# Performance work log

Measured on AMD Instinct MI355X. Metric: run time of the kernel, lower is better.

## Reference

```python
import jax, jax.numpy as jnp
import numpy as np

DEPTH, BREADTH, N_HEADS = 6, 1024, 16
D_HEAD = BREADTH // N_HEADS
EPS = 1e-5


def layer_norm(x, g, b):
    m = jnp.mean(x, axis=-1, keepdims=True)
    v = jnp.mean(jnp.square(x - m), axis=-1, keepdims=True)
    return (x - m) * jax.lax.rsqrt(v + EPS) * g + b


def setup_inputs() -> dict:
    key = jax.random.key(0)
    ks = jax.random.split(key, 16)
    B, S, Dm, Dff = 4, 1024, BREADTH, 4 * BREADTH
    s = 0.02
    return {
        "x": jax.random.normal(ks[0], (B, S, Dm), dtype=jnp.float32),
        "mask": jnp.ones((B, S, S), dtype=jnp.int32),
        "wq": s * jax.random.normal(ks[1], (DEPTH, Dm, Dm), dtype=jnp.float32),
        "bq": jnp.zeros((DEPTH, Dm), dtype=jnp.float32),
        "wk": s * jax.random.normal(ks[2], (DEPTH, Dm, Dm), dtype=jnp.float32),
        "bk": jnp.zeros((DEPTH, Dm), dtype=jnp.float32),
        "wv": s * jax.random.normal(ks[3], (DEPTH, Dm, Dm), dtype=jnp.float32),
        "bv": jnp.zeros((DEPTH, Dm), dtype=jnp.float32),
        "wo": s * jax.random.normal(ks[4], (DEPTH, Dm, Dm), dtype=jnp.float32),
        "bo": jnp.zeros((DEPTH, Dm), dtype=jnp.float32),
        "w1": s * jax.random.normal(ks[5], (DEPTH, Dm, Dff), dtype=jnp.float32),
        "b1": jnp.zeros((DEPTH, Dff), dtype=jnp.float32),
        "w2": s * jax.random.normal(ks[6], (DEPTH, Dff, Dm), dtype=jnp.float32),
        "b2": jnp.zeros((DEPTH, Dm), dtype=jnp.float32),
        "ln1g": jnp.ones((DEPTH, Dm), dtype=jnp.float32),
        "ln1b": jnp.zeros((DEPTH, Dm), dtype=jnp.float32),
        "ln2g": jnp.ones((DEPTH, Dm), dtype=jnp.float32),
        "ln2b": jnp.zeros((DEPTH, Dm), dtype=jnp.float32),
        "lnfg": jnp.ones((Dm,), dtype=jnp.float32),
        "lnfb": jnp.zeros((Dm,), dtype=jnp.float32),
    }


def reference(x, mask, wq, bq, wk, bk, wv, bv, wo, bo, w1, b1, w2, b2,
              ln1g, ln1b, ln2g, ln2b, lnfg, lnfb):
    B, S, Dm = x.shape
    scale = 1.0 / jnp.sqrt(jnp.float32(D_HEAD))
    neg = jnp.float32(-1e9)
    mask_b = (mask == 0)[:, None]  # [B,1,S,S]

    def split_heads(t):  # [B,S,Dm] -> [B,H,S,d]
        return t.reshape(B, S, N_HEADS, D_HEAD).transpose(0, 2, 1, 3)

    for i in range(DEPTH):
        xn1 = layer_norm(x, ln1g[i], ln1b[i])  # attention branch input
        xn2 = layer_norm(x, ln2g[i], ln2b[i])  # FFN branch input (pre-attention, per original)

        q = split_heads(xn1 @ wq[i] + bq[i])
        k = split_heads(xn1 @ wk[i] + bk[i])
        v = split_heads(xn1 @ wv[i] + bv[i])
        scores = jnp.einsum("bhqd,bhkd->bhqk", q, k) * scale
        scores = jnp.where(mask_b, neg, scores)
        attn = jax.nn.softmax(scores, axis=-1)
        ctx = jnp.einsum("bhqk,bhkd->bhqd", attn, v)
        ctx = ctx.transpose(0, 2, 1, 3).reshape(B, S, Dm)
        x = x + (ctx @ wo[i] + bo[i])

        h = jax.nn.relu(xn2 @ w1[i] + b1[i])
        x = x + (h @ w2[i] + b2[i])

    return layer_norm(x, lnfg, lnfb)
```

## Files before the change

### kernel.cpp

```cpp
#include <hip/hip_runtime.h>
#include <hip/hip_bf16.h>
#include <stdint.h>

#define DEPTH 6
#define DM 1024
#define DFF 4096
#define NH 16
#define DH 64
#define BATCH 4
#define SEQ 1024
#define NTOK (BATCH*SEQ)
#define QKVLD 3072

using bf16x8 = __attribute__((ext_vector_type(8))) short;
using f32x4  = __attribute__((ext_vector_type(4))) float;
typedef unsigned short u16;

__device__ __forceinline__ u16 f2bf(float f) {
  union { float f; uint32_t u; } v; v.f = f;
  return (u16)((v.u + 0x7FFFu + ((v.u >> 16) & 1u)) >> 16);
}

__device__ __forceinline__ void async16(void* lds, const void* g) {
  __builtin_amdgcn_global_load_lds(
      (__attribute__((address_space(1))) void*)(unsigned long long)g,
      (__attribute__((address_space(3))) void*)(unsigned int)(unsigned long long)lds,
      16, 0, 0);
}

__global__ __launch_bounds__(256)
void prep(const float* __restrict__ wq, const float* __restrict__ wk,
          const float* __restrict__ wv, const float* __restrict__ wo,
          const float* __restrict__ w1, const float* __restrict__ w2,
          const float* __restrict__ bq, const float* __restrict__ bk,
          const float* __restrict__ bv,
          u16* __restrict__ wqkvT, u16* __restrict__ woT,
          u16* __restrict__ w1T, u16* __restrict__ w2T,
          float* __restrict__ bqkv) {
  const int bid = blockIdx.x;
  if (bid >= 12288) {
    const int t = (bid - 12288) * 256 + threadIdx.x;
    bqkv[t] = t < 1024 ? bq[t] : (t < 2048 ? bk[t - 1024] : bv[t - 2048]);
    return;
  }
  const float* w; u16* wt; int K, N, tile;
  if (bid < 3072)      { const int r = bid >> 10;
                         w = r == 0 ? wq : (r == 1 ? wk : wv);
                         wt = wqkvT + (size_t)r * 1024 * 1024; K = 1024; N = 1024; tile = bid & 1023; }
  else if (bid < 4096) { w = wo; wt = woT; K = 1024; N = 1024; tile = bid - 3072; }
  else if (bid < 8192) { w = w1; wt = w1T; K = 1024; N = 4096; tile = bid - 4096; }
  else                 { w = w2; wt = w2T; K = 4096; N = 1024; tile = bid - 8192; }
  const int ntn = N >> 5;
  const int k0 = (tile / ntn) << 5, n0 = (tile % ntn) << 5;

  __shared__ u16 t[32][33];
  const int tx = threadIdx.x & 31, ty = threadIdx.x >> 5;
  #pragma unroll
  for (int r = ty; r < 32; r += 8)
    t[r][tx] = f2bf(w[(size_t)(k0 + r) * N + n0 + tx]);
  __syncthreads();
  #pragma unroll
  for (int r = ty; r < 32; r += 8)
    wt[(size_t)(n0 + r) * K + k0 + tx] = t[tx][r];
}

__global__ __launch_bounds__(256)
void vtrans(const u16* __restrict__ qkv, u16* __restrict__ vt) {
  __shared__ u16 t[64][72];
  const int s0 = blockIdx.x * 64, c0 = blockIdx.y * 64, b = blockIdx.z;
  const int r = threadIdx.x >> 2, cq = threadIdx.x & 3;
  const u16* src = qkv + ((size_t)(b * SEQ + s0 + r)) * QKVLD + 2048 + c0 + cq * 16;
  *(bf16x8*)&t[r][cq * 16]     = *(const bf16x8*)(src);
  *(bf16x8*)&t[r][cq * 16 + 8] = *(const bf16x8*)(src + 8);
  __syncthreads();
  bf16x8 a, bvec;
  #pragma unroll
  for (int i = 0; i < 8; i++) a[i] = (short)t[cq * 16 + i][r];
  #pragma unroll
  for (int i = 0; i < 8; i++) bvec[i] = (short)t[cq * 16 + 8 + i][r];
  u16* dst = vt + ((size_t)(b * 1024 + c0 + r)) * SEQ + s0 + cq * 16;
  *(bf16x8*)dst = a;
  *(bf16x8*)(dst + 8) = bvec;
}

__global__ void flags_init(int* flags) {
  if (threadIdx.x < BATCH) flags[threadIdx.x] = 1;
}
__global__ void mask_flags(const int* __restrict__ mask, int* __restrict__ flags) {
  const size_t n = (size_t)BATCH * SEQ * SEQ;
  for (size_t i = (size_t)blockIdx.x * 256 + threadIdx.x; i < n; i += (size_t)gridDim.x * 256)
    if (mask[i] == 0) flags[i / ((size_t)SEQ * SEQ)] = 0;
}

__global__ __launch_bounds__(256)
void ln_dual(const float* __restrict__ x,
             const float* __restrict__ g1, const float* __restrict__ b1v,
             const float* __restrict__ g2, const float* __restrict__ b2v,
             u16* __restrict__ o1, u16* __restrict__ o2) {
  const int row = blockIdx.x, tid = threadIdx.x;
  const float4 v = ((const float4*)(x + (size_t)row * DM))[tid];
  float s = v.x + v.y + v.z + v.w;
  float sq = v.x*v.x + v.y*v.y + v.z*v.z + v.w*v.w;
  #pragma unroll
  for (int o = 32; o; o >>= 1) { s += __shfl_xor(s, o); sq += __shfl_xor(sq, o); }
  __shared__ float red[8];
  const int lane = tid & 63, w = tid >> 6;
  if (lane == 0) { red[w] = s; red[4 + w] = sq; }
  __syncthreads();
  s = red[0] + red[1] + red[2] + red[3];
  sq = red[4] + red[5] + red[6] + red[7];
  const float mean = s * (1.0f / DM);
  const float rinv = rsqrtf(sq * (1.0f / DM) - mean * mean + 1e-5f);
  const float4 G1 = ((const float4*)g1)[tid], B1 = ((const float4*)b1v)[tid];
  const float4 G2 = ((const float4*)g2)[tid], B2 = ((const float4*)b2v)[tid];
  const float n0 = (v.x - mean) * rinv, n1 = (v.y - mean) * rinv;
  const float n2 = (v.z - mean) * rinv, n3 = (v.w - mean) * rinv;
  ushort4 a, bb;
  a.x = f2bf(n0*G1.x + B1.x); a.y = f2bf(n1*G1.y + B1.y);
  a.z = f2bf(n2*G1.z + B1.z); a.w = f2bf(n3*G1.w + B1.w);
  bb.x = f2bf(n0*G2.x + B2.x); bb.y = f2bf(n1*G2.y + B2.y);
  bb.z = f2bf(n2*G2.z + B2.z); bb.w = f2bf(n3*G2.w + B2.w);
  ((ushort4*)(o1 + (size_t)row * DM))[tid] = a;
  ((ushort4*)(o2 + (size_t)row * DM))[tid] = bb;
}

__global__ __launch_bounds__(256)
void ln_final(const float* __restrict__ x, const float* __restrict__ g,
              const float* __restrict__ b, float* __restrict__ out) {
  const int row = blockIdx.x, tid = threadIdx.x;
  const float4 v = ((const float4*)(x + (size_t)row * DM))[tid];
  float s = v.x + v.y + v.z + v.w;
  float sq = v.x*v.x + v.y*v.y + v.z*v.z + v.w*v.w;
  #pragma unroll
  for (int o = 32; o; o >>= 1) { s += __shfl_xor(s, o); sq += __shfl_xor(sq, o); }
  __shared__ float red[8];
  const int lane = tid & 63, w = tid >> 6;
  if (lane == 0) { red[w] = s; red[4 + w] = sq; }
  __syncthreads();
  s = red[0] + red[1] + red[2] + red[3];
  sq = red[4] + red[5] + red[6] + red[7];
  const float mean = s * (1.0f / DM);
  const float rinv = rsqrtf(sq * (1.0f / DM) - mean * mean + 1e-5f);
  const float4 G = ((const float4*)g)[tid], B = ((const float4*)b)[tid];
  float4 o;
  o.x = (v.x - mean) * rinv * G.x + B.x;
  o.y = (v.y - mean) * rinv * G.y + B.y;
  o.z = (v.z - mean) * rinv * G.z + B.z;
  o.w = (v.w - mean) * rinv * G.w + B.w;
  ((float4*)(out + (size_t)row * DM))[tid] = o;
}

template<int EPI, int BN>
__global__ __launch_bounds__(256)
void gemm_bt(const u16* __restrict__ A, const u16* __restrict__ BT,
             const float* __restrict__ bias,
             u16* __restrict__ Cb, float* __restrict__ Cf,
             int M, int N, int K) {
  constexpr int WCn = BN / 64;
  constexpr int WR  = 4 / WCn;
  constexpr int MF  = 8 / WR;
  constexpr int WRS = 128 / WR;
  constexpr int ASZ = 128 * 32;
  constexpr int BSZ = BN * 32;
  __shared__ u16 As[2 * ASZ];
  __shared__ u16 Bs[2 * BSZ];
  const int tid = threadIdx.x;
  const int lane = tid & 63, wave = tid >> 6;
  const int wr = wave / WCn, wc = wave % WCn;
  const int l16 = lane & 15, lhi = lane >> 4;

  const int ntn = N / BN;
  const int nwg = (M >> 7) * ntn;
  int wg = (int)blockIdx.x;
  if ((nwg & 7) == 0) { const int q = nwg >> 3; wg = (wg & 7) * q + (wg >> 3); }
  const int tm = wg / ntn, tn = wg % ntn;

  const int srow = tid >> 2, sc = (tid & 3) * 8;
  const u16* Ag0 = A  + (size_t)(tm * 128 + srow) * K + sc;
  const u16* Bg0 = BT + (size_t)(tn * BN + srow) * K + sc;
  const size_t rstep = (size_t)64 * K;

  auto stage = [&](int buf, int k0) {
    async16(As + buf * ASZ + tid * 8, Ag0 + k0);
    async16(As + buf * ASZ + 2048 + tid * 8, Ag0 + rstep + k0);
    async16(Bs + buf * BSZ + tid * 8, Bg0 + k0);
    if constexpr (BN == 128) async16(Bs + buf * BSZ + 2048 + tid * 8, Bg0 + rstep + k0);
  };

  f32x4 acc[MF][4];
  #pragma unroll
  for (int m = 0; m < MF; m++)
    #pragma unroll
    for (int n = 0; n < 4; n++)
      #pragma unroll
      for (int j = 0; j < 4; j++) acc[m][n][j] = 0.0f;

  stage(0, 0);
  __syncthreads();
  int cur = 0;
  for (int k0 = 0; k0 < K; k0 += 32) {
    if (k0 + 32 < K) stage(cur ^ 1, k0 + 32);
    const u16* Ab = As + cur * ASZ;
    const u16* Bb = Bs + cur * BSZ;
    bf16x8 af[MF], bfv[4];
    #pragma unroll
    for (int m = 0; m < MF; m++)
      af[m] = *(const bf16x8*)&Ab[(wr * WRS + m * 16 + l16) * 32 + lhi * 8];
    #pragma unroll
    for (int n = 0; n < 4; n++)
      bfv[n] = *(const bf16x8*)&Bb[(wc * 64 + n * 16 + l16) * 32 + lhi * 8];
    #pragma unroll
    for (int m = 0; m < MF; m++)
      #pragma unroll
      for (int n = 0; n < 4; n++)
        acc[m][n] = __builtin_amdgcn_mfma_f32_16x16x32_bf16(af[m], bfv[n], acc[m][n], 0, 0, 0);
    __syncthreads();
    cur ^= 1;
  }

  const int row0 = tm * 128 + wr * WRS + lhi * 4;
  const int col0 = tn * BN + wc * 64 + l16;
  #pragma unroll
  for (int n = 0; n < 4; n++) {
    const int col = col0 + n * 16;
    const float bv = bias[col];
    #pragma unroll
    for (int m = 0; m < MF; m++) {
      #pragma unroll
      for (int j = 0; j < 4; j++) {
        const int row = row0 + m * 16 + j;
        float v = acc[m][n][j] + bv;
        if constexpr (EPI == 1) v = fmaxf(v, 0.0f);
        if constexpr (EPI <= 1) Cb[(size_t)row * N + col] = f2bf(v);
        else                    Cf[(size_t)row * N + col] += v;
      }
    }
  }
}

__global__ __launch_bounds__(256, 4)
void attn(const u16* __restrict__ QKV, const u16* __restrict__ VTg,
          u16* __restrict__ Octx,
          const int* __restrict__ mask, const int* __restrict__ flags) {
  __shared__ u16 Ks[2 * 64 * 64];
  __shared__ u16 VTs[2 * 64 * 64];
  __shared__ u16 Ps[4 * 16 * 64];
  const int tid = threadIdx.x, lane = tid & 63, wv = tid >> 6;
  const int l16 = lane & 15, lhi = lane >> 4;
  const int bid = blockIdx.x;
  const int pair = bid >> 4, qblk = bid & 15;
  const int b = pair >> 4, h = pair & 15;
  const int hoff = h * DH;
  const int q0 = qblk * 64 + wv * 16;
  const size_t tokbase = (size_t)b * SEQ;
  const size_t vbase = ((size_t)b * 1024 + hoff) * SEQ;

  bf16x8 qf[2];
  #pragma unroll
  for (int ds = 0; ds < 2; ds++)
    qf[ds] = *(const bf16x8*)&QKV[(tokbase + q0 + l16) * QKVLD + hoff + ds * 32 + lhi * 8];

  f32x4 oacc[4];
  #pragma unroll
  for (int nt = 0; nt < 4; nt++)
    #pragma unroll
    for (int j = 0; j < 4; j++) oacc[nt][j] = 0.0f;
  float mrun = -1e30f, lrun = 0.0f;

  const int allone = flags[b];
  char* PwB = (char*)(Ps + wv * (16 * 64));
  const int xw = (l16 & 7) << 4;

  const int srow0 = tid >> 3, scb0 = (tid & 7) ^ (srow0 & 7);
  const int srow1 = (tid + 256) >> 3, scb1 = (tid & 7) ^ (srow1 & 7);
  const int shfl_src = (lane & 48) + ((lane >> 4) << 2);

  auto stage = [&](int buf, int kt) {
    async16((char*)Ks + buf * 8192 + tid * 16,
            &QKV[(tokbase + kt + srow0) * QKVLD + 1024 + hoff + scb0 * 8]);
    async16((char*)Ks + buf * 8192 + 4096 + tid * 16,
            &QKV[(tokbase + kt + srow1) * QKVLD + 1024 + hoff + scb1 * 8]);
    async16((char*)VTs + buf * 8192 + tid * 16,
            &VTg[vbase + (size_t)srow0 * SEQ + kt + scb0 * 8]);
    async16((char*)VTs + buf * 8192 + 4096 + tid * 16,
            &VTg[vbase + (size_t)srow1 * SEQ + kt + scb1 * 8]);
  };

  stage(0, 0);
  __syncthreads();
  int cur = 0;
  for (int kt = 0; kt < SEQ; kt += 64) {
    if (kt + 64 < SEQ) stage(cur ^ 1, kt + 64);
    char* KsB = (char*)Ks + cur * 8192;
    char* VTB = (char*)VTs + cur * 8192;

    f32x4 sacc[4];
    #pragma unroll
    for (int nt = 0; nt < 4; nt++)
      #pragma unroll
      for (int j = 0; j < 4; j++) sacc[nt][j] = 0.0f;
    #pragma unroll
    for (int ds = 0; ds < 2; ds++) {
      bf16x8 kf[4];
      #pragma unroll
      for (int nt = 0; nt < 4; nt++) {
        const int rk = nt * 16 + l16;
        kf[nt] = *(const bf16x8*)(KsB + ((rk * 128 + ds * 64 + lhi * 16) ^ ((rk & 7) << 4)));
      }
      #pragma unroll
      for (int nt = 0; nt < 4; nt++)
        sacc[nt] = __builtin_amdgcn_mfma_f32_16x16x32_bf16(kf[nt], qf[ds], sacc[nt], 0, 0, 0);
    }
    #pragma unroll
    for (int nt = 0; nt < 4; nt++)
      #pragma unroll
      for (int j = 0; j < 4; j++) sacc[nt][j] *= 0.125f;

    if (!allone) {
      const int qg = q0 + l16;
      #pragma unroll
      for (int nt = 0; nt < 4; nt++)
        #pragma unroll
        for (int j = 0; j < 4; j++) {
          const int kc = kt + nt * 16 + lhi * 4 + j;
          if (mask[(tokbase + qg) * SEQ + kc] == 0) sacc[nt][j] = -1e9f;
        }
    }

    float tmax = -1e30f;
    #pragma unroll
    for (int nt = 0; nt < 4; nt++)
      #pragma unroll
      for (int j = 0; j < 4; j++) tmax = fmaxf(tmax, sacc[nt][j]);
    tmax = fmaxf(tmax, __shfl_xor(tmax, 16));
    tmax = fmaxf(tmax, __shfl_xor(tmax, 32));
    const float mnew = fmaxf(mrun, tmax);
    const float corr = __expf(mrun - mnew);
    float p[4][4];
    float tsum = 0.0f;
    #pragma unroll
    for (int nt = 0; nt < 4; nt++)
      #pragma unroll
      for (int j = 0; j < 4; j++) { p[nt][j] = __expf(sacc[nt][j] - mnew); tsum += p[nt][j]; }
    tsum += __shfl_xor(tsum, 16);
    tsum += __shfl_xor(tsum, 32);
    lrun = lrun * corr + tsum;
    mrun = mnew;

    #pragma unroll
    for (int nt = 0; nt < 4; nt++) {
      const uint32_t lo = (uint32_t)f2bf(p[nt][0]) | ((uint32_t)f2bf(p[nt][1]) << 16);
      const uint32_t hi = (uint32_t)f2bf(p[nt][2]) | ((uint32_t)f2bf(p[nt][3]) << 16);
      *(uint64_t*)(PwB + ((l16 * 128 + nt * 32 + lhi * 8) ^ xw)) =
          (uint64_t)lo | ((uint64_t)hi << 32);
    }

    float cj[4];
    #pragma unroll
    for (int j = 0; j < 4; j++) cj[j] = __shfl(corr, shfl_src + j);
    #pragma unroll
    for (int nt = 0; nt < 4; nt++)
      #pragma unroll
      for (int j = 0; j < 4; j++) oacc[nt][j] *= cj[j];

    #pragma unroll
    for (int ksl = 0; ksl < 2; ksl++) {
      const bf16x8 pf = *(const bf16x8*)(PwB + ((l16 * 128 + ksl * 64 + lhi * 16) ^ xw));
      #pragma unroll
      for (int nt = 0; nt < 4; nt++) {
        const int dr = nt * 16 + l16;
        const bf16x8 vf = *(const bf16x8*)(VTB + ((dr * 128 + ksl * 64 + lhi * 16) ^ ((dr & 7) << 4)));
        oacc[nt] = __builtin_amdgcn_mfma_f32_16x16x32_bf16(pf, vf, oacc[nt], 0, 0, 0);
      }
    }
    __syncthreads();
    cur ^= 1;
  }

  const float linv = 1.0f / lrun;
  float lj[4];
  #pragma unroll
  for (int j = 0; j < 4; j++) lj[j] = __shfl(linv, shfl_src + j);
  #pragma unroll
  for (int j = 0; j < 4; j++) {
    const size_t rowg = (tokbase + q0 + lhi * 4 + j) * DM + hoff;
    #pragma unroll
    for (int nt = 0; nt < 4; nt++)
      Octx[rowg + nt * 16 + l16] = f2bf(oacc[nt][j] * lj[j]);
  }
}

extern "C" void kernel_launch(void* const* d_in, const int* in_sizes, int n_in,
                              void* d_out, int out_size, void* d_ws, size_t ws_size,
                              hipStream_t stream) {
  const float* x    = (const float*)d_in[0];
  const int*   mask = (const int*)d_in[1];
  const float* wq = (const float*)d_in[2];
  const float* bq = (const float*)d_in[3];
  const float* wk = (const float*)d_in[4];
  const float* bk = (const float*)d_in[5];
  const float* wvp = (const float*)d_in[6];
  const float* bv = (const float*)d_in[7];
  const float* wo = (const float*)d_in[8];
  const float* bo = (const float*)d_in[9];
  const float* w1 = (const float*)d_in[10];
  const float* b1 = (const float*)d_in[11];
  const float* w2 = (const float*)d_in[12];
  const float* b2 = (const float*)d_in[13];
  const float* ln1g = (const float*)d_in[14];
  const float* ln1b = (const float*)d_in[15];
  const float* ln2g = (const float*)d_in[16];
  const float* ln2b = (const float*)d_in[17];
  const float* lnfg = (const float*)d_in[18];
  const float* lnfb = (const float*)d_in[19];

  char* ws = (char*)d_ws;
  float* xbuf = (float*)(ws);
  u16* xn1  = (u16*)(ws + ((size_t)16 << 20));
  u16* xn2  = (u16*)(ws + ((size_t)24 << 20));
  u16* qkv  = (u16*)(ws + ((size_t)32 << 20));
  u16* ctx  = (u16*)(ws + ((size_t)56 << 20));
  u16* hb   = (u16*)(ws + ((size_t)32 << 20));
  u16* wqkvT= (u16*)(ws + ((size_t)64 << 20));
  u16* woT  = (u16*)(ws + ((size_t)70 << 20));
  u16* w1T  = (u16*)(ws + ((size_t)72 << 20));
  u16* w2T  = (u16*)(ws + ((size_t)80 << 20));
  u16* vT   = (u16*)(ws + ((size_t)88 << 20));
  float* bqkv = (float*)(ws + ((size_t)96 << 20));
  int* flags  = (int*)(ws + ((size_t)96 << 20) + 65536);

  hipMemcpyAsync(xbuf, x, (size_t)NTOK * DM * sizeof(float),
                 hipMemcpyDeviceToDevice, stream);
  flags_init<<<1, 64, 0, stream>>>(flags);
  mask_flags<<<1024, 256, 0, stream>>>(mask, flags);

  auto wgs128 = [](int M, int N) { return dim3((unsigned)((M >> 7) * (N >> 7))); };
  auto wgs64  = [](int M, int N) { return dim3((unsigned)((M >> 7) * (N >> 6))); };

  for (int i = 0; i < DEPTH; i++) {
    prep<<<12300, 256, 0, stream>>>(
        wq  + (size_t)i * DM * DM,  wk + (size_t)i * DM * DM,
        wvp + (size_t)i * DM * DM,  wo + (size_t)i * DM * DM,
        w1  + (size_t)i * DM * DFF, w2 + (size_t)i * DFF * DM,
        bq + i * DM, bk + i * DM, bv + i * DM,
        wqkvT, woT, w1T, w2T, bqkv);

    ln_dual<<<NTOK, 256, 0, stream>>>(xbuf, ln1g + i * DM, ln1b + i * DM,
                                      ln2g + i * DM, ln2b + i * DM, xn1, xn2);

    gemm_bt<0, 128><<<wgs128(NTOK, QKVLD), 256, 0, stream>>>(xn1, wqkvT, bqkv, qkv, nullptr,
                                                             NTOK, QKVLD, DM);
    vtrans<<<dim3(16, 16, 4), 256, 0, stream>>>(qkv, vT);

    attn<<<1024, 256, 0, stream>>>(qkv, vT, ctx, mask, flags);

    gemm_bt<2, 64><<<wgs64(NTOK, DM), 256, 0, stream>>>(ctx, woT, bo + i * DM, nullptr, xbuf,
                                                        NTOK, DM, DM);
    gemm_bt<1, 128><<<wgs128(NTOK, DFF), 256, 0, stream>>>(xn2, w1T, b1 + i * DFF, hb, nullptr,
                                                           NTOK, DFF, DM);
    gemm_bt<2, 64><<<wgs64(NTOK, DM), 256, 0, stream>>>(hb, w2T, b2 + i * DM, nullptr, xbuf,
                                                        NTOK, DM, DFF);
  }

  ln_final<<<NTOK, 256, 0, stream>>>(xbuf, lnfg, lnfb, (float*)d_out);
}
```

Before: 1.523 ms.

## Add 256x256 tiled bf16 GEMM with split-K atomics for QKV and FFN layers

Introduces a new 512-thread GEMM kernel with 256x256 output tiles, a swizzled LDS layout, double-buffered async global-to-LDS loads, interleaved MFMA phases with priority hints, and XCD-aware workgroup remapping. It replaces the 128-tile GEMMs for the QKV and FFN-up projections. The FFN-down projection now uses 4-way split-K with float atomic adds into the residual buffer. The larger tiles aim to raise arithmetic intensity and cut global and LDS traffic per MFMA. In exchange, atomic accumulation makes the floating-point sum order nondeterministic, and register pressure from the 8x4 accumulator tile is high.

After: 1.591 ms. +4.4%, slower.

```diff
diff --git a/kernel.cpp b/kernel.cpp
--- a/kernel.cpp
+++ b/kernel.cpp
@@ -27,6 +27,8 @@
       (__attribute__((address_space(3))) void*)(unsigned int)(unsigned long long)lds,
       16, 0, 0);
 }
+
+#define BARRIER() do { __builtin_amdgcn_s_barrier(); asm volatile("" ::: "memory"); } while (0)
 
 __global__ __launch_bounds__(256)
 void prep(const float* __restrict__ wq, const float* __restrict__ wk,
@@ -148,6 +150,176 @@
   o.z = (v.z - mean) * rinv * G.z + B.z;
   o.w = (v.w - mean) * rinv * G.w + B.w;
   ((float4*)(out + (size_t)row * DM))[tid] = o;
+}
+
+template<int EPI, int SPLITK>
+__global__ __launch_bounds__(512, 2)
+void gemm256(const u16* __restrict__ A, const u16* __restrict__ BT,
+             const float* __restrict__ bias,
+             u16* __restrict__ Cb, float* __restrict__ Cf,
+             int M, int N, int K) {
+  __shared__ u16 lds[65536];
+  char* ldsb = (char*)lds;
+  const int tid = threadIdx.x;
+  const int lane = tid & 63;
+  const int wid = tid >> 6;
+  const int wm = wid >> 2, wn = wid & 3;
+  const int l16 = lane & 15, lhi = lane >> 4;
+  const int xr = (l16 & 7) << 4;
+
+  const int ntn = N >> 8;
+  const int ntiles = (M >> 8) * ntn;
+  const int nwg = ntiles * SPLITK;
+  int wg = (int)blockIdx.x;
+  if ((nwg & 7) == 0) { const int q = nwg >> 3; wg = (wg & 7) * q + (wg >> 3); }
+  const int ks = wg / ntiles;
+  const int tile = wg % ntiles;
+  const int tm = tile / ntn, tn = tile % ntn;
+  const int KS = K / SPLITK;
+  const int k0 = ks * KS;
+  const int NT = KS >> 6;
+
+  const u16 *aS[4], *bS[4];
+  #pragma unroll
+  for (int g = 0; g < 4; g++) {
+    const int D  = tid * 16 + g * 8192;
+    const int Dh = D & 16383, half = D >> 14;
+    const int Ds = Dh ^ (((Dh >> 7) & 7) << 4);
+    const int grow = half * 128 + (Ds >> 7);
+    const int gcol = (Ds & 127) >> 1;
+    aS[g] = A  + (size_t)(tm * 256 + grow) * K + k0 + gcol;
+    bS[g] = BT + (size_t)(tn * 256 + grow) * K + k0 + gcol;
+  }
+  auto stageA = [&](int buf, int t) {
+    #pragma unroll
+    for (int g = 0; g < 4; g++)
+      async16(ldsb + buf * 32768 + g * 8192 + tid * 16, aS[g] + t * 64);
+  };
+  auto stageB = [&](int buf, int t) {
+    #pragma unroll
+    for (int g = 0; g < 4; g++)
+      async16(ldsb + 65536 + buf * 32768 + g * 8192 + tid * 16, bS[g] + t * 64);
+  };
+  auto ldA = [&](int buf, int mq, int m, int kk) -> bf16x8 {
+    const int L = (mq * 64 + m * 16 + l16) * 128 + kk * 64 + lhi * 16;
+    return *(const bf16x8*)(ldsb + buf * 32768 + wm * 16384 + (L ^ xr));
+  };
+  auto ldB = [&](int buf, int nq, int n, int kk) -> bf16x8 {
+    const int L = ((wn & 1) * 64 + nq * 32 + n * 16 + l16) * 128 + kk * 64 + lhi * 16;
+    return *(const bf16x8*)(ldsb + 65536 + buf * 32768 + (wn >> 1) * 16384 + (L ^ xr));
+  };
+
+  f32x4 acc[8][4];
+  #pragma unroll
+  for (int m = 0; m < 8; m++)
+    #pragma unroll
+    for (int n = 0; n < 4; n++)
+      #pragma unroll
+      for (int j = 0; j < 4; j++) acc[m][n][j] = 0.0f;
+
+  stageA(0, 0); stageB(0, 0);
+  stageA(1, 1); stageB(1, 1);
+  asm volatile("s_waitcnt vmcnt(8)" ::: "memory");
+  BARRIER();
+
+  bf16x8 a[4][2], b0[2][2], b1[2][2];
+  for (int t = 0; t < NT; ++t) {
+    const int buf = t & 1;
+    #pragma unroll
+    for (int m = 0; m < 4; m++)
+      #pragma unroll
+      for (int kk = 0; kk < 2; kk++) a[m][kk] = ldA(buf, 0, m, kk);
+    #pragma unroll
+    for (int n = 0; n < 2; n++)
+      #pragma unroll
+      for (int kk = 0; kk < 2; kk++) b0[n][kk] = ldB(buf, 0, n, kk);
+    BARRIER();
+    asm volatile("s_waitcnt lgkmcnt(0)" ::: "memory");
+    __builtin_amdgcn_s_setprio(1);
+    #pragma unroll
+    for (int m = 0; m < 4; m++)
+      #pragma unroll
+      for (int n = 0; n < 2; n++)
+        #pragma unroll
+        for (int kk = 0; kk < 2; kk++)
+          acc[m][n] = __builtin_amdgcn_mfma_f32_16x16x32_bf16(a[m][kk], b0[n][kk], acc[m][n], 0, 0, 0);
+    __builtin_amdgcn_s_setprio(0);
+    BARRIER();
+    #pragma unroll
+    for (int n = 0; n < 2; n++)
+      #pragma unroll
+      for (int kk = 0; kk < 2; kk++) b1[n][kk] = ldB(buf, 1, n, kk);
+    BARRIER();
+    asm volatile("s_waitcnt lgkmcnt(0)" ::: "memory");
+    __builtin_amdgcn_s_setprio(1);
+    #pragma unroll
+    for (int m = 0; m < 4; m++)
+      #pragma unroll
+      for (int n = 0; n < 2; n++)
+        #pragma unroll
+        for (int kk = 0; kk < 2; kk++)
+          acc[m][2 + n] = __builtin_amdgcn_mfma_f32_16x16x32_bf16(a[m][kk], b1[n][kk], acc[m][2 + n], 0, 0, 0);
+    __builtin_amdgcn_s_setprio(0);
+    BARRIER();
+    #pragma unroll
+    for (int m = 0; m < 4; m++)
+      #pragma unroll
+      for (int kk = 0; kk < 2; kk++) a[m][kk] = ldA(buf, 1, m, kk);
+    if (t + 2 < NT) stageB(buf, t + 2);
+    BARRIER();
+    asm volatile("s_waitcnt lgkmcnt(0)" ::: "memory");
+    __builtin_amdgcn_s_setprio(1);
+    #pragma unroll
+    for (int m = 0; m < 4; m++)
+      #pragma unroll
+      for (int n = 0; n < 2; n++)
+        #pragma unroll
+        for (int kk = 0; kk < 2; kk++)
+          acc[4 + m][2 + n] = __builtin_amdgcn_mfma_f32_16x16x32_bf16(a[m][kk], b1[n][kk], acc[4 + m][2 + n], 0, 0, 0);
+    __builtin_amdgcn_s_setprio(0);
+    BARRIER();
+    if (t + 2 < NT) stageA(buf, t + 2);
+    BARRIER();
+    __builtin_amdgcn_s_setprio(1);
+    #pragma unroll
+    for (int m = 0; m < 4; m++)
+      #pragma unroll
+      for (int n = 0; n < 2; n++)
+        #pragma unroll
+        for (int kk = 0; kk < 2; kk++)
+          acc[4 + m][n] = __builtin_amdgcn_mfma_f32_16x16x32_bf16(a[m][kk], b0[n][kk], acc[4 + m][n], 0, 0, 0);
+    __builtin_amdgcn_s_setprio(0);
+    if (t + 1 < NT) {
+      if (t + 2 < NT) asm volatile("s_waitcnt vmcnt(8)" ::: "memory");
+      else            asm volatile("s_waitcnt vmcnt(0)" ::: "memory");
+      BARRIER();
+    }
+  }
+
+  const int row0 = tm * 256 + wm * 128 + lhi * 4;
+  const int col0 = tn * 256 + wn * 64 + l16;
+  #pragma unroll
+  for (int ng = 0; ng < 4; ng++) {
+    const int col = col0 + ng * 16;
+    const float bv = bias[col];
+    #pragma unroll
+    for (int mg = 0; mg < 8; mg++) {
+      #pragma unroll
+      for (int j = 0; j < 4; j++) {
+        const int row = row0 + mg * 16 + j;
+        float v = acc[mg][ng][j];
+        if constexpr (EPI == 2 && SPLITK > 1) {
+          if (ks == 0) v += bv;
+          unsafeAtomicAdd(&Cf[(size_t)row * N + col], v);
+        } else {
+          v += bv;
+          if constexpr (EPI == 1) v = fmaxf(v, 0.0f);
+          if constexpr (EPI <= 1) Cb[(size_t)row * N + col] = f2bf(v);
+          else                    Cf[(size_t)row * N + col] += v;
+        }
+      }
+    }
+  }
 }
 
 template<int EPI, int BN>
@@ -434,8 +606,7 @@
   flags_init<<<1, 64, 0, stream>>>(flags);
   mask_flags<<<1024, 256, 0, stream>>>(mask, flags);
 
-  auto wgs128 = [](int M, int N) { return dim3((unsigned)((M >> 7) * (N >> 7))); };
-  auto wgs64  = [](int M, int N) { return dim3((unsigned)((M >> 7) * (N >> 6))); };
+  auto wgs64 = [](int M, int N) { return dim3((unsigned)((M >> 7) * (N >> 6))); };
 
   for (int i = 0; i < DEPTH; i++) {
     prep<<<12300, 256, 0, stream>>>(
@@ -448,18 +619,18 @@
     ln_dual<<<NTOK, 256, 0, stream>>>(xbuf, ln1g + i * DM, ln1b + i * DM,
                                       ln2g + i * DM, ln2b + i * DM, xn1, xn2);
 
-    gemm_bt<0, 128><<<wgs128(NTOK, QKVLD), 256, 0, stream>>>(xn1, wqkvT, bqkv, qkv, nullptr,
-                                                             NTOK, QKVLD, DM);
+    gemm256<0, 1><<<dim3(192), 512, 0, stream>>>(xn1, wqkvT, bqkv, qkv, nullptr,
+                                                 NTOK, QKVLD, DM);
     vtrans<<<dim3(16, 16, 4), 256, 0, stream>>>(qkv, vT);
 
     attn<<<1024, 256, 0, stream>>>(qkv, vT, ctx, mask, flags);
 
     gemm_bt<2, 64><<<wgs64(NTOK, DM), 256, 0, stream>>>(ctx, woT, bo + i * DM, nullptr, xbuf,
                                                         NTOK, DM, DM);
-    gemm_bt<1, 128><<<wgs128(NTOK, DFF), 256, 0, stream>>>(xn2, w1T, b1 + i * DFF, hb, nullptr,
-                                                           NTOK, DFF, DM);
-    gemm_bt<2, 64><<<wgs64(NTOK, DM), 256, 0, stream>>>(hb, w2T, b2 + i * DM, nullptr, xbuf,
-                                                        NTOK, DM, DFF);
+    gemm256<1, 1><<<dim3(256), 512, 0, stream>>>(xn2, w1T, b1 + i * DFF, hb, nullptr,
+                                                 NTOK, DFF, DM);
+    gemm256<2, 4><<<dim3(256), 512, 0, stream>>>(hb, w2T, b2 + i * DM, nullptr, xbuf,
+                                                 NTOK, DM, DFF);
   }
 
   ln_final<<<NTOK, 256, 0, stream>>>(xbuf, lnfg, lnfb, (float*)d_out);
```

## Split-K the W2 GEMM and fold the partial sum into the next layernorm

Applied to the files above, without the earlier changes.

The FFN down-projection (K=4096) is split into two K halves, which doubles the workgroup count from 512 to 1024. The first half adds its result plus bias into the residual buffer, and the second half writes a separate fp32 slab. The next ln_dual, or ln_final after the last layer, adds the slab into the residual before normalising and writes the sum back. This is meant to improve occupancy on a tile-count-limited GEMM, at the cost of writing and reading an extra 16MB fp32 slab per layer. The split path only runs if the workspace is large enough.

New measurement: 1.520 ms (median of 2 runs). About the same (-0.2%).

```diff
diff --git a/kernel.cpp b/kernel.cpp
--- a/kernel.cpp
+++ b/kernel.cpp
@@ -93,12 +93,17 @@
 }
 
 __global__ __launch_bounds__(256)
-void ln_dual(const float* __restrict__ x,
+void ln_dual(float* __restrict__ x, const float* __restrict__ slab,
              const float* __restrict__ g1, const float* __restrict__ b1v,
              const float* __restrict__ g2, const float* __restrict__ b2v,
              u16* __restrict__ o1, u16* __restrict__ o2) {
   const int row = blockIdx.x, tid = threadIdx.x;
-  const float4 v = ((const float4*)(x + (size_t)row * DM))[tid];
+  float4 v = ((const float4*)(x + (size_t)row * DM))[tid];
+  if (slab) {
+    const float4 sv = ((const float4*)(slab + (size_t)row * DM))[tid];
+    v.x += sv.x; v.y += sv.y; v.z += sv.z; v.w += sv.w;
+    ((float4*)(x + (size_t)row * DM))[tid] = v;
+  }
   float s = v.x + v.y + v.z + v.w;
   float sq = v.x*v.x + v.y*v.y + v.z*v.z + v.w*v.w;
   #pragma unroll
@@ -125,10 +130,15 @@
 }
 
 __global__ __launch_bounds__(256)
-void ln_final(const float* __restrict__ x, const float* __restrict__ g,
-              const float* __restrict__ b, float* __restrict__ out) {
+void ln_final(const float* __restrict__ x, const float* __restrict__ slab,
+              const float* __restrict__ g, const float* __restrict__ b,
+              float* __restrict__ out) {
   const int row = blockIdx.x, tid = threadIdx.x;
-  const float4 v = ((const float4*)(x + (size_t)row * DM))[tid];
+  float4 v = ((const float4*)(x + (size_t)row * DM))[tid];
+  if (slab) {
+    const float4 sv = ((const float4*)(slab + (size_t)row * DM))[tid];
+    v.x += sv.x; v.y += sv.y; v.z += sv.z; v.w += sv.w;
+  }
   float s = v.x + v.y + v.z + v.w;
   float sq = v.x*v.x + v.y*v.y + v.z*v.z + v.w*v.w;
   #pragma unroll
@@ -150,11 +160,11 @@
   ((float4*)(out + (size_t)row * DM))[tid] = o;
 }
 
-template<int EPI, int BN>
+template<int EPI, int BN, int SPLITK>
 __global__ __launch_bounds__(256)
 void gemm_bt(const u16* __restrict__ A, const u16* __restrict__ BT,
              const float* __restrict__ bias,
-             u16* __restrict__ Cb, float* __restrict__ Cf,
+             u16* __restrict__ Cb, float* __restrict__ Cf, float* __restrict__ Cf2,
              int M, int N, int K) {
   constexpr int WCn = BN / 64;
   constexpr int WR  = 4 / WCn;
@@ -170,14 +180,17 @@
   const int l16 = lane & 15, lhi = lane >> 4;
 
   const int ntn = N / BN;
-  const int nwg = (M >> 7) * ntn;
+  const int ntiles = (M >> 7) * ntn;
+  const int nwg = ntiles * SPLITK;
   int wg = (int)blockIdx.x;
   if ((nwg & 7) == 0) { const int q = nwg >> 3; wg = (wg & 7) * q + (wg >> 3); }
-  const int tm = wg / ntn, tn = wg % ntn;
+  const int tile = wg / SPLITK, ks = wg % SPLITK;
+  const int tm = tile / ntn, tn = tile % ntn;
+  const int KL = K / SPLITK;
 
   const int srow = tid >> 2, sc = (tid & 3) * 8;
-  const u16* Ag0 = A  + (size_t)(tm * 128 + srow) * K + sc;
-  const u16* Bg0 = BT + (size_t)(tn * BN + srow) * K + sc;
+  const u16* Ag0 = A  + (size_t)(tm * 128 + srow) * K + ks * KL + sc;
+  const u16* Bg0 = BT + (size_t)(tn * BN + srow) * K + ks * KL + sc;
   const size_t rstep = (size_t)64 * K;
 
   auto stage = [&](int buf, int k0) {
@@ -198,8 +211,8 @@
   stage(0, 0);
   __syncthreads();
   int cur = 0;
-  for (int k0 = 0; k0 < K; k0 += 32) {
-    if (k0 + 32 < K) stage(cur ^ 1, k0 + 32);
+  for (int k0 = 0; k0 < KL; k0 += 32) {
+    if (k0 + 32 < KL) stage(cur ^ 1, k0 + 32);
     const u16* Ab = As + cur * ASZ;
     const u16* Bb = Bs + cur * BSZ;
     bf16x8 af[MF], bfv[4];
@@ -229,10 +242,17 @@
       #pragma unroll
       for (int j = 0; j < 4; j++) {
         const int row = row0 + m * 16 + j;
-        float v = acc[m][n][j] + bv;
-        if constexpr (EPI == 1) v = fmaxf(v, 0.0f);
-        if constexpr (EPI <= 1) Cb[(size_t)row * N + col] = f2bf(v);
-        else                    Cf[(size_t)row * N + col] += v;
+        const size_t idx = (size_t)row * N + col;
+        float v = acc[m][n][j];
+        if constexpr (EPI == 3) {
+          if (ks == 0) Cf[idx] += v + bv;
+          else         Cf2[idx] = v;
+        } else {
+          v += bv;
+          if constexpr (EPI == 1) v = fmaxf(v, 0.0f);
+          if constexpr (EPI <= 1) Cb[idx] = f2bf(v);
+          else                    Cf[idx] += v;
+        }
       }
     }
   }
@@ -428,6 +448,9 @@
   u16* vT   = (u16*)(ws + ((size_t)88 << 20));
   float* bqkv = (float*)(ws + ((size_t)96 << 20));
   int* flags  = (int*)(ws + ((size_t)96 << 20) + 65536);
+  float* slab = (float*)(ws + ((size_t)97 << 20));
+
+  const bool splitw2 = ws_size >= ((size_t)113 << 20);
 
   hipMemcpyAsync(xbuf, x, (size_t)NTOK * DM * sizeof(float),
                  hipMemcpyDeviceToDevice, stream);
@@ -445,22 +468,30 @@
         bq + i * DM, bk + i * DM, bv + i * DM,
         wqkvT, woT, w1T, w2T, bqkv);
 
-    ln_dual<<<NTOK, 256, 0, stream>>>(xbuf, ln1g + i * DM, ln1b + i * DM,
+    ln_dual<<<NTOK, 256, 0, stream>>>(xbuf, (splitw2 && i > 0) ? slab : nullptr,
+                                      ln1g + i * DM, ln1b + i * DM,
                                       ln2g + i * DM, ln2b + i * DM, xn1, xn2);
 
-    gemm_bt<0, 128><<<wgs128(NTOK, QKVLD), 256, 0, stream>>>(xn1, wqkvT, bqkv, qkv, nullptr,
-                                                             NTOK, QKVLD, DM);
+    gemm_bt<0, 128, 1><<<wgs128(NTOK, QKVLD), 256, 0, stream>>>(
+        xn1, wqkvT, bqkv, qkv, nullptr, nullptr, NTOK, QKVLD, DM);
     vtrans<<<dim3(16, 16, 4), 256, 0, stream>>>(qkv, vT);
 
     attn<<<1024, 256, 0, stream>>>(qkv, vT, ctx, mask, flags);
 
-    gemm_bt<2, 64><<<wgs64(NTOK, DM), 256, 0, stream>>>(ctx, woT, bo + i * DM, nullptr, xbuf,
-                                                        NTOK, DM, DM);
-    gemm_bt<1, 128><<<wgs128(NTOK, DFF), 256, 0, stream>>>(xn2, w1T, b1 + i * DFF, hb, nullptr,
-                                                           NTOK, DFF, DM);
-    gemm_bt<2, 64><<<wgs64(NTOK, DM), 256, 0, stream>>>(hb, w2T, b2 + i * DM, nullptr, xbuf,
-                                                        NTOK, DM, DFF);
-  }
-
-  ln_final<<<NTOK, 256, 0, stream>>>(xbuf, lnfg, lnfb, (float*)d_out);
-}
+    gemm_bt<2, 64, 1><<<wgs64(NTOK, DM), 256, 0, stream>>>(
+        ctx, woT, bo + i * DM, nullptr, xbuf, nullptr, NTOK, DM, DM);
+    gemm_bt<1, 128, 1><<<wgs128(NTOK, DFF), 256, 0, stream>>>(
+        xn2, w1T, b1 + i * DFF, hb, nullptr, nullptr, NTOK, DFF, DM);
+
+    if (splitw2) {
+      gemm_bt<3, 64, 2><<<dim3((NTOK >> 7) * (DM >> 6) * 2), 256, 0, stream>>>(
+          hb, w2T, b2 + i * DM, nullptr, xbuf, slab, NTOK, DM, DFF);
+    } else {
+      gemm_bt<2, 64, 1><<<wgs64(NTOK, DM), 256, 0, stream>>>(
+          hb, w2T, b2 + i * DM, nullptr, xbuf, nullptr, NTOK, DM, DFF);
+    }
+  }
+
+  ln_final<<<NTOK, 256, 0, stream>>>(xbuf, splitw2 ? slab : nullptr,
+                                     lnfg, lnfb, (float*)d_out);
+}
```

## Split-K the output-projection and FFN-down GEMMs with atomic accumulation

Applied to the files above, without the earlier changes.

Adds a SPLITK template parameter to the GEMM so each workgroup covers only a slice of K, and adds an epilogue that accumulates into the fp32 residual with atomics. Bias is added only by the first slice. The Wo projection uses 2 splits and the FFN-down projection uses 4. Before this, those two N=1024 GEMMs launched only 512 workgroups, and the FFN-down one also ran a long K loop. Splitting raises workgroup count and shortens per-workgroup latency, at the cost of more atomic traffic and a summation order that is no longer deterministic.

After: 1.754 ms. +15.1%, slower.

```diff
diff --git a/kernel.cpp b/kernel.cpp
--- a/kernel.cpp
+++ b/kernel.cpp
@@ -150,7 +150,7 @@
   ((float4*)(out + (size_t)row * DM))[tid] = o;
 }
 
-template<int EPI, int BN>
+template<int EPI, int BN, int SPLITK>
 __global__ __launch_bounds__(256)
 void gemm_bt(const u16* __restrict__ A, const u16* __restrict__ BT,
              const float* __restrict__ bias,
@@ -170,14 +170,17 @@
   const int l16 = lane & 15, lhi = lane >> 4;
 
   const int ntn = N / BN;
-  const int nwg = (M >> 7) * ntn;
+  const int ntiles = (M >> 7) * ntn;
+  const int nwg = ntiles * SPLITK;
   int wg = (int)blockIdx.x;
   if ((nwg & 7) == 0) { const int q = nwg >> 3; wg = (wg & 7) * q + (wg >> 3); }
-  const int tm = wg / ntn, tn = wg % ntn;
+  const int tile = wg / SPLITK, ks = wg % SPLITK;
+  const int tm = tile / ntn, tn = tile % ntn;
+  const int KL = K / SPLITK;
 
   const int srow = tid >> 2, sc = (tid & 3) * 8;
-  const u16* Ag0 = A  + (size_t)(tm * 128 + srow) * K + sc;
-  const u16* Bg0 = BT + (size_t)(tn * BN + srow) * K + sc;
+  const u16* Ag0 = A  + (size_t)(tm * 128 + srow) * K + ks * KL + sc;
+  const u16* Bg0 = BT + (size_t)(tn * BN + srow) * K + ks * KL + sc;
   const size_t rstep = (size_t)64 * K;
 
   auto stage = [&](int buf, int k0) {
@@ -198,8 +201,8 @@
   stage(0, 0);
   __syncthreads();
   int cur = 0;
-  for (int k0 = 0; k0 < K; k0 += 32) {
-    if (k0 + 32 < K) stage(cur ^ 1, k0 + 32);
+  for (int k0 = 0; k0 < KL; k0 += 32) {
+    if (k0 + 32 < KL) stage(cur ^ 1, k0 + 32);
     const u16* Ab = As + cur * ASZ;
     const u16* Bb = Bs + cur * BSZ;
     bf16x8 af[MF], bfv[4];
@@ -229,10 +232,17 @@
       #pragma unroll
       for (int j = 0; j < 4; j++) {
         const int row = row0 + m * 16 + j;
-        float v = acc[m][n][j] + bv;
-        if constexpr (EPI == 1) v = fmaxf(v, 0.0f);
-        if constexpr (EPI <= 1) Cb[(size_t)row * N + col] = f2bf(v);
-        else                    Cf[(size_t)row * N + col] += v;
+        const size_t idx = (size_t)row * N + col;
+        float v = acc[m][n][j];
+        if constexpr (EPI == 4) {
+          if (ks == 0) v += bv;
+          unsafeAtomicAdd(&Cf[idx], v);
+        } else {
+          v += bv;
+          if constexpr (EPI == 1) v = fmaxf(v, 0.0f);
+          if constexpr (EPI <= 1) Cb[idx] = f2bf(v);
+          else                    Cf[idx] += v;
+        }
       }
     }
   }
@@ -435,7 +445,6 @@
   mask_flags<<<1024, 256, 0, stream>>>(mask, flags);
 
   auto wgs128 = [](int M, int N) { return dim3((unsigned)((M >> 7) * (N >> 7))); };
-  auto wgs64  = [](int M, int N) { return dim3((unsigned)((M >> 7) * (N >> 6))); };
 
   for (int i = 0; i < DEPTH; i++) {
     prep<<<12300, 256, 0, stream>>>(
@@ -448,18 +457,20 @@
     ln_dual<<<NTOK, 256, 0, stream>>>(xbuf, ln1g + i * DM, ln1b + i * DM,
                                       ln2g + i * DM, ln2b + i * DM, xn1, xn2);
 
-    gemm_bt<0, 128><<<wgs128(NTOK, QKVLD), 256, 0, stream>>>(xn1, wqkvT, bqkv, qkv, nullptr,
-                                                             NTOK, QKVLD, DM);
+    gemm_bt<0, 128, 1><<<wgs128(NTOK, QKVLD), 256, 0, stream>>>(
+        xn1, wqkvT, bqkv, qkv, nullptr, NTOK, QKVLD, DM);
     vtrans<<<dim3(16, 16, 4), 256, 0, stream>>>(qkv, vT);
 
     attn<<<1024, 256, 0, stream>>>(qkv, vT, ctx, mask, flags);
 
-    gemm_bt<2, 64><<<wgs64(NTOK, DM), 256, 0, stream>>>(ctx, woT, bo + i * DM, nullptr, xbuf,
-                                                        NTOK, DM, DM);
-    gemm_bt<1, 128><<<wgs128(NTOK, DFF), 256, 0, stream>>>(xn2, w1T, b1 + i * DFF, hb, nullptr,
-                                                           NTOK, DFF, DM);
-    gemm_bt<2, 64><<<wgs64(NTOK, DM), 256, 0, stream>>>(hb, w2T, b2 + i * DM, nullptr, xbuf,
-                                                        NTOK, DM, DFF);
+    gemm_bt<4, 64, 2><<<dim3((NTOK >> 7) * (DM >> 6) * 2), 256, 0, stream>>>(
+        ctx, woT, bo + i * DM, nullptr, xbuf, NTOK, DM, DM);
+
+    gemm_bt<1, 128, 1><<<wgs128(NTOK, DFF), 256, 0, stream>>>(
+        xn2, w1T, b1 + i * DFF, hb, nullptr, NTOK, DFF, DM);
+
+    gemm_bt<4, 64, 4><<<dim3((NTOK >> 7) * (DM >> 6) * 4), 256, 0, stream>>>(
+        hb, w2T, b2 + i * DM, nullptr, xbuf, NTOK, DM, DFF);
   }
 
   ln_final<<<NTOK, 256, 0, stream>>>(xbuf, lnfg, lnfb, (float*)d_out);
```
